# Optimization experiments

Measured on AMD Instinct MI355X. Metric: run time of the kernel, lower is better.

The kernel has to match this reference:

```python
import jax, jax.numpy as jnp
import numpy as np

MIN_TOKENS_RATIO = 0.25
WARMUP_STEPS = 1000
THRESH_SENS = 0.5


def _difficulty(logits, targets):
    # logits: (N, V) float, targets: (N,) int. All under stop_gradient by caller.
    V = logits.shape[-1]
    logp = jax.nn.log_softmax(logits, axis=-1)
    p = jnp.exp(logp)
    entropy = -jnp.sum(p * logp, axis=-1)                      # (N,)
    top2 = jax.lax.top_k(p, 2)[0]                              # (N, 2)
    confidence = top2[..., 0]
    margin = top2[..., 0] - top2[..., 1]
    ce = -jnp.take_along_axis(logp, targets[:, None], axis=-1)[:, 0]
    ent_norm = entropy / jnp.log(jnp.asarray(V, logits.dtype))
    loss_norm = ce / (jnp.max(ce) + 1e-6)
    # 'combined' scoring: mean of normalized entropy, inverted margin, normalized loss
    difficulty = (ent_norm + (1.0 - margin) + loss_norm) / 3.0
    return difficulty, confidence


def setup_inputs() -> dict:
    key = jax.random.key(0)
    k1, k2 = jax.random.split(key)
    B, S, V = 4, 2048, 32000
    logits = jax.random.normal(k1, (B, S, V), dtype=jnp.float32)
    targets = jax.random.randint(k2, (B, S), 0, V)
    return {"logits": logits, "targets": targets, "step_count": 1000}


def reference(logits, targets, step_count):
    B, S, V = logits.shape
    N = B * S
    lf = logits.reshape(N, V)
    tf = targets.reshape(N)

    # --- no-grad difficulty scoring (torch.no_grad analogue) ---
    difficulty, confidence = _difficulty(jax.lax.stop_gradient(lf), tf)

    # linear curriculum from 1.0 to min_tokens_ratio
    progress = min(1.0, float(step_count) / WARMUP_STEPS)
    base_ratio = 1.0 - progress * (1.0 - MIN_TOKENS_RATIO)

    # dynamic threshold: keep more tokens when batch confidence is low
    avg_conf = jnp.mean(confidence)
    ratio = jnp.clip(base_ratio * (1.0 + THRESH_SENS * (0.5 - avg_conf) * 2.0), 0.01, 1.0)

    # top-k hardest tokens via dynamic threshold on sorted difficulty (jit-safe: static shapes)
    k = jnp.clip(jnp.round(ratio * N).astype(jnp.int32), 1, N)
    sorted_d = jnp.sort(difficulty)            # ascending
    threshold = sorted_d[N - k]                # k-th largest value
    mask = (difficulty >= threshold).astype(lf.dtype)

    # --- masked CE over selected tokens (differentiable path) ---
    logp = jax.nn.log_softmax(lf, axis=-1)
    ce = -jnp.take_along_axis(logp, tf[:, None], axis=-1)[:, 0]
    loss = jnp.sum(ce * mask) / jnp.maximum(jnp.sum(mask), 1.0)
    return loss
```

## Files before the change

### kernel.cpp

```cpp
#include <hip/hip_runtime.h>
#include <math.h>

#define NROWS 8192
#define VDIM  32000
#define V4    (VDIM / 4)
#define LOG_V 10.373491181781864f

__device__ __forceinline__ void sm_combine(float &m, float &l2, float &s, float &t,
                                           float m2, float l22, float s2, float t2) {
    float M  = fmaxf(m, m2);
    float L2 = fmaxf(fminf(m, m2), fmaxf(l2, l22));
    float c1 = __expf(m  - M);
    float c2 = __expf(m2 - M);
    float T  = c1 * (t + s * (m - M)) + c2 * (t2 + s2 * (m2 - M));
    float S  = c1 * s + c2 * s2;
    m = M; l2 = L2; s = S; t = T;
}

__global__ __launch_bounds__(256) void row_stats_kernel(
    const float* __restrict__ logits, const int* __restrict__ targets,
    float* __restrict__ ce_out, float* __restrict__ dp_out,
    float* __restrict__ conf_out)
{
    const int r   = blockIdx.x;
    const int tid = threadIdx.x;
    const float4* row = reinterpret_cast<const float4*>(logits + (size_t)r * VDIM);

    float m = -1e30f, l2 = -1e30f, s = 0.0f, t = 0.0f;

    for (int i = tid; i < V4; i += 256) {
        float4 v = row[i];
        float xs[4] = {v.x, v.y, v.z, v.w};
#pragma unroll
        for (int j = 0; j < 4; ++j) {
            float x = xs[j];
            if (x > m) {
                float c = __expf(m - x);
                t = (t + s * (m - x)) * c;
                s = fmaf(s, c, 1.0f);
                l2 = m;
                m = x;
            } else {
                float d = __expf(x - m);
                l2 = fmaxf(l2, x);
                s += d;
                t = fmaf(d, x - m, t);
            }
        }
    }

#pragma unroll
    for (int mask = 1; mask < 64; mask <<= 1) {
        float m2  = __shfl_xor(m,  mask, 64);
        float l22 = __shfl_xor(l2, mask, 64);
        float s2  = __shfl_xor(s,  mask, 64);
        float t2  = __shfl_xor(t,  mask, 64);
        sm_combine(m, l2, s, t, m2, l22, s2, t2);
    }

    __shared__ float red[4][4];
    const int wave = tid >> 6;
    const int lane = tid & 63;
    if (lane == 0) { red[wave][0] = m; red[wave][1] = l2; red[wave][2] = s; red[wave][3] = t; }
    __syncthreads();
    if (tid == 0) {
        for (int w = 1; w < 4; ++w)
            sm_combine(m, l2, s, t, red[w][0], red[w][1], red[w][2], red[w][3]);
        float lt    = logits[(size_t)r * VDIM + targets[r]];
        float logs  = __logf(s);
        float inv_s = 1.0f / s;
        float ce     = (m - lt) + logs;
        float ent    = logs - t * inv_s;
        float conf   = inv_s;
        float margin = (1.0f - __expf(l2 - m)) * inv_s;
        ce_out[r]   = ce;
        dp_out[r]   = ent * (1.0f / LOG_V) + (1.0f - margin);
        conf_out[r] = conf;
    }
}

__global__ __launch_bounds__(1024) void finalize_kernel(
    const float* __restrict__ ce_arr, const float* __restrict__ dp_arr,
    const float* __restrict__ conf_arr, const int* __restrict__ step_count,
    float* __restrict__ out)
{
    __shared__ float sortbuf[NROWS];
    __shared__ float wredA[16], wredB[16];
    __shared__ float s_bc[2];
    __shared__ float s_th;

    const int tid  = threadIdx.x;
    const int wave = tid >> 6;
    const int lane = tid & 63;

    float mx = -1e30f, sc = 0.0f;
    for (int i = tid; i < NROWS; i += 1024) {
        mx = fmaxf(mx, ce_arr[i]);
        sc += conf_arr[i];
    }
#pragma unroll
    for (int mask = 1; mask < 64; mask <<= 1) {
        mx = fmaxf(mx, __shfl_xor(mx, mask, 64));
        sc += __shfl_xor(sc, mask, 64);
    }
    if (lane == 0) { wredA[wave] = mx; wredB[wave] = sc; }
    __syncthreads();
    if (tid == 0) {
        float M = wredA[0], S = wredB[0];
        for (int w = 1; w < 16; ++w) { M = fmaxf(M, wredA[w]); S += wredB[w]; }
        s_bc[0] = M + 1e-6f;
        s_bc[1] = S * (1.0f / (float)NROWS);
    }
    __syncthreads();
    const float denom = s_bc[0];

    for (int i = tid; i < NROWS; i += 1024)
        sortbuf[i] = (dp_arr[i] + ce_arr[i] / denom) * (1.0f / 3.0f);
    __syncthreads();

    for (int k = 2; k <= NROWS; k <<= 1) {
        for (int j = k >> 1; j > 0; j >>= 1) {
            for (int i = tid; i < NROWS; i += 1024) {
                int ixj = i ^ j;
                if (ixj > i) {
                    float a = sortbuf[i], b = sortbuf[ixj];
                    if ((a > b) == ((i & k) == 0)) { sortbuf[i] = b; sortbuf[ixj] = a; }
                }
            }
            __syncthreads();
        }
    }

    if (tid == 0) {
        float progress   = fminf(1.0f, (float)step_count[0] * (1.0f / 1000.0f));
        float base_ratio = 1.0f - progress * 0.75f;
        float avg_conf   = s_bc[1];
        float ratio = base_ratio * (1.0f + 0.5f * (0.5f - avg_conf) * 2.0f);
        ratio = fminf(fmaxf(ratio, 0.01f), 1.0f);
        int kk = (int)rintf(ratio * (float)NROWS);
        kk = kk < 1 ? 1 : (kk > NROWS ? NROWS : kk);
        s_th = sortbuf[NROWS - kk];
    }
    __syncthreads();
    const float th = s_th;

    float msum = 0.0f, mcnt = 0.0f;
    for (int i = tid; i < NROWS; i += 1024) {
        float ce = ce_arr[i];
        float d  = (dp_arr[i] + ce / denom) * (1.0f / 3.0f);
        if (d >= th) { msum += ce; mcnt += 1.0f; }
    }
#pragma unroll
    for (int mask = 1; mask < 64; mask <<= 1) {
        msum += __shfl_xor(msum, mask, 64);
        mcnt += __shfl_xor(mcnt, mask, 64);
    }
    __syncthreads();
    if (lane == 0) { wredA[wave] = msum; wredB[wave] = mcnt; }
    __syncthreads();
    if (tid == 0) {
        float S = 0.0f, C = 0.0f;
        for (int w = 0; w < 16; ++w) { S += wredA[w]; C += wredB[w]; }
        out[0] = S / fmaxf(C, 1.0f);
    }
}

extern "C" void kernel_launch(void* const* d_in, const int* in_sizes, int n_in,
                              void* d_out, int out_size, void* d_ws, size_t ws_size,
                              hipStream_t stream) {
    const float* logits  = (const float*)d_in[0];
    const int*   targets = (const int*)d_in[1];
    const int*   step    = (const int*)d_in[2];
    float* ws = (float*)d_ws;
    float* ce = ws;
    float* dp = ws + NROWS;
    float* cf = ws + 2 * NROWS;

    row_stats_kernel<<<NROWS, 256, 0, stream>>>(logits, targets, ce, dp, cf);
    finalize_kernel<<<1, 1024, 0, stream>>>(ce, dp, cf, step, (float*)d_out);
}
```

Baseline: 1.381 ms.

## Replace bitonic sort with radix select and unroll row loads

The finalize kernel no longer bitonic-sorts all 8192 difficulty scores in shared memory. It finds the k-th largest value with a four-pass, 8-bit radix select over order-preserving unsigned keys, using shared-memory histograms, and caches CE values in shared memory. The row-stats kernel also issues four float4 loads per iteration before processing them, to raise memory-level parallelism. The radix select relies on the key transform to preserve float ordering, and does serial histogram scans on a single thread.

```diff
diff --git a/kernel.cpp b/kernel.cpp
--- a/kernel.cpp
+++ b/kernel.cpp
@@ -28,8 +28,7 @@
 
     float m = -1e30f, l2 = -1e30f, s = 0.0f, t = 0.0f;
 
-    for (int i = tid; i < V4; i += 256) {
-        float4 v = row[i];
+    auto proc = [&](float4 v) {
         float xs[4] = {v.x, v.y, v.z, v.w};
 #pragma unroll
         for (int j = 0; j < 4; ++j) {
@@ -47,7 +46,17 @@
                 t = fmaf(d, x - m, t);
             }
         }
-    }
+    };
+
+    int i = tid;
+    for (; i + 768 < V4; i += 1024) {
+        float4 a = row[i];
+        float4 b = row[i + 256];
+        float4 c = row[i + 512];
+        float4 d = row[i + 768];
+        proc(a); proc(b); proc(c); proc(d);
+    }
+    for (; i < V4; i += 256) proc(row[i]);
 
 #pragma unroll
     for (int mask = 1; mask < 64; mask <<= 1) {
@@ -84,10 +93,13 @@
     const float* __restrict__ conf_arr, const int* __restrict__ step_count,
     float* __restrict__ out)
 {
-    __shared__ float sortbuf[NROWS];
+    __shared__ unsigned keys[NROWS];
+    __shared__ float    s_ce[NROWS];
+    __shared__ unsigned hist[256];
     __shared__ float wredA[16], wredB[16];
     __shared__ float s_bc[2];
-    __shared__ float s_th;
+    __shared__ unsigned s_prefix;
+    __shared__ int s_krem;
 
     const int tid  = threadIdx.x;
     const int wave = tid >> 6;
@@ -95,13 +107,15 @@
 
     float mx = -1e30f, sc = 0.0f;
     for (int i = tid; i < NROWS; i += 1024) {
-        mx = fmaxf(mx, ce_arr[i]);
+        float ce = ce_arr[i];
+        s_ce[i] = ce;
+        mx = fmaxf(mx, ce);
         sc += conf_arr[i];
     }
 #pragma unroll
-    for (int mask = 1; mask < 64; mask <<= 1) {
-        mx = fmaxf(mx, __shfl_xor(mx, mask, 64));
-        sc += __shfl_xor(sc, mask, 64);
+    for (int msk = 1; msk < 64; msk <<= 1) {
+        mx = fmaxf(mx, __shfl_xor(mx, msk, 64));
+        sc += __shfl_xor(sc, msk, 64);
     }
     if (lane == 0) { wredA[wave] = mx; wredB[wave] = sc; }
     __syncthreads();
@@ -114,23 +128,11 @@
     __syncthreads();
     const float denom = s_bc[0];
 
-    for (int i = tid; i < NROWS; i += 1024)
-        sortbuf[i] = (dp_arr[i] + ce_arr[i] / denom) * (1.0f / 3.0f);
-    __syncthreads();
-
-    for (int k = 2; k <= NROWS; k <<= 1) {
-        for (int j = k >> 1; j > 0; j >>= 1) {
-            for (int i = tid; i < NROWS; i += 1024) {
-                int ixj = i ^ j;
-                if (ixj > i) {
-                    float a = sortbuf[i], b = sortbuf[ixj];
-                    if ((a > b) == ((i & k) == 0)) { sortbuf[i] = b; sortbuf[ixj] = a; }
-                }
-            }
-            __syncthreads();
-        }
-    }
-
+    for (int i = tid; i < NROWS; i += 1024) {
+        float d = (dp_arr[i] + s_ce[i] / denom) * (1.0f / 3.0f);
+        unsigned u = __float_as_uint(d);
+        keys[i] = (u & 0x80000000u) ? ~u : (u | 0x80000000u);
+    }
     if (tid == 0) {
         float progress   = fminf(1.0f, (float)step_count[0] * (1.0f / 1000.0f));
         float base_ratio = 1.0f - progress * 0.75f;
@@ -139,21 +141,51 @@
         ratio = fminf(fmaxf(ratio, 0.01f), 1.0f);
         int kk = (int)rintf(ratio * (float)NROWS);
         kk = kk < 1 ? 1 : (kk > NROWS ? NROWS : kk);
-        s_th = sortbuf[NROWS - kk];
-    }
-    __syncthreads();
-    const float th = s_th;
+        s_krem = kk;
+        s_prefix = 0u;
+    }
+    __syncthreads();
+
+    unsigned hi_mask = 0u;
+#pragma unroll
+    for (int shift = 24; shift >= 0; shift -= 8) {
+        if (tid < 256) hist[tid] = 0u;
+        __syncthreads();
+        const unsigned pfx = s_prefix;
+        for (int i = tid; i < NROWS; i += 1024) {
+            unsigned u = keys[i];
+            if ((u & hi_mask) == pfx)
+                atomicAdd(&hist[(u >> shift) & 255u], 1u);
+        }
+        __syncthreads();
+        if (tid == 0) {
+            int krem = s_krem;
+            unsigned c = 0;
+            int sel = -1;
+            int rem = 0;
+            for (int b = 255; b >= 0; --b) {
+                unsigned h = hist[b];
+                unsigned cnew = c + h;
+                bool hit = ((int)cnew >= krem) && (sel < 0);
+                if (hit) { sel = b; rem = krem - (int)c; }
+                c = cnew;
+            }
+            s_krem   = rem;
+            s_prefix = pfx | ((unsigned)sel << shift);
+        }
+        __syncthreads();
+        hi_mask |= (0xFFu << shift);
+    }
+    const unsigned kth = s_prefix;
 
     float msum = 0.0f, mcnt = 0.0f;
     for (int i = tid; i < NROWS; i += 1024) {
-        float ce = ce_arr[i];
-        float d  = (dp_arr[i] + ce / denom) * (1.0f / 3.0f);
-        if (d >= th) { msum += ce; mcnt += 1.0f; }
-    }
-#pragma unroll
-    for (int mask = 1; mask < 64; mask <<= 1) {
-        msum += __shfl_xor(msum, mask, 64);
-        mcnt += __shfl_xor(mcnt, mask, 64);
+        if (keys[i] >= kth) { msum += s_ce[i]; mcnt += 1.0f; }
+    }
+#pragma unroll
+    for (int msk = 1; msk < 64; msk <<= 1) {
+        msum += __shfl_xor(msum, msk, 64);
+        mcnt += __shfl_xor(mcnt, msk, 64);
     }
     __syncthreads();
     if (lane == 0) { wredA[wave] = msum; wredB[wave] = mcnt; }
```

Measured after the change: 1.335 ms. 3.3% less time.
